# Kernel tuning notes

Measured on AMD Instinct MI355X. Metric: run time of the kernel, lower is better.

The kernel has to match this reference:

```python
import jax, jax.numpy as jnp
import numpy as np

IN_DIM, OUT_DIM = 96, 32
D = IN_DIM + OUT_DIM  # 128, feature dim of x
H, KQ = 8, 64         # head_num, KQ_dim
GAMMA = 1e-4


def setup_inputs() -> dict:
    key = jax.random.key(0)
    kx, kk, kq, kv = jax.random.split(key, 4)
    B, N = 32, 2048
    std_kq = (GAMMA / D) ** 0.5
    return {
        "x": jax.random.normal(kx, (B, N, D), dtype=jnp.float32),
        # nn.Linear weight shape [out_features, in_features]; stacked per head
        "Wk": jax.random.normal(kk, (H, KQ, D), dtype=jnp.float32) * std_kq,
        "Wq": jax.random.normal(kq, (H, KQ, D), dtype=jnp.float32) * std_kq,
        "Wv": jax.random.normal(kv, (H, D, D), dtype=jnp.float32) * GAMMA,
    }


def reference(x, Wk, Wq, Wv):
    # Per-head projections (nn.Linear: y = x @ W^T), stacked over heads h
    K = jnp.einsum("bnd,hkd->bhnk", x, Wk)  # [B,H,N,KQ]
    Q = jnp.einsum("bnd,hkd->bhnk", x, Wq)  # [B,H,N,KQ]
    V = jnp.einsum("bnd,hed->bhne", x, Wv)  # [B,H,N,D]
    # No softmax -> (Q K^T) V == Q (K^T V); use the O(n d^2) associative form
    KtV = jnp.einsum("bhnk,bhne->bhke", K, V)  # [B,H,KQ,D]
    # sum over heads folded into the contraction
    out = jnp.einsum("bhnk,bhke->bne", Q, KtV)  # [B,N,D]
    return out
```

## Files before the change

kernel.cpp:

```cpp
#include <hip/hip_runtime.h>

#define BB 32
#define NN 2048
#define DD 128
#define HH 8
#define KK 64

typedef __attribute__((ext_vector_type(8))) short bf16x8;
typedef __attribute__((ext_vector_type(4))) float f32x4;
#define MFMA_BF16 __builtin_amdgcn_mfma_f32_16x16x32_bf16


__device__ __forceinline__ float bf2f(unsigned short h){ return __uint_as_float(((unsigned)h) << 16); }
__device__ __forceinline__ unsigned short f2bf(float f){
  unsigned u = __float_as_uint(f);
  u += 0x7fffu + ((u >> 16) & 1u);
  return (unsigned short)(u >> 16);
}
__device__ __forceinline__ unsigned pack2(float a, float b){
  return (unsigned)f2bf(a) | ((unsigned)f2bf(b) << 16);
}

__device__ __forceinline__ bf16x8 ldfrag_sw(const unsigned short* base, int row16, int kc, int lane){
  int d = row16 + (lane & 15);
  int q = lane >> 4;
  int ch = ((kc << 2) + q) ^ (d & 7);
  return *(const bf16x8*)(base + d*128 + ch*8);
}

__global__ __launch_bounds__(512, 4) void kgkp(const float* __restrict__ x,
                                               const float* __restrict__ Wq,
                                               const float* __restrict__ Wk,
                                               unsigned short* __restrict__ Gp_bf,
                                               unsigned short* __restrict__ Pbf,
                                               unsigned short* __restrict__ x_bf){
  __shared__ __align__(16) unsigned short sm[32768];
  const int t = threadIdx.x;
  const int bid = blockIdx.x;
  const int w = t >> 6, lane = t & 63, quad = lane >> 4;
  if (bid < 256){
    unsigned short* xh = sm;
    unsigned short* xl = sm + 16384;
    const int b = bid & 31, chunk = bid >> 5;
    const int wr = (w >> 1)*32, wc = (w & 1)*64;
    f32x4 acc[2][4] = {};
    for (int sub = 0; sub < 2; ++sub){
      if (sub) __syncthreads();
      const float* xb = x + ((size_t)b*NN + (size_t)(chunk*256 + sub*128))*DD;
      unsigned short* xbo = x_bf + (((size_t)(b*16 + chunk*2 + sub)) << 14);
      for (int it = 0; it < 2; ++it){
        int gidx = it*512 + t;
        int n4g = (gidx & 7) | (((gidx >> 6) & 3) << 3);
        int dcq = ((gidx >> 3) & 7) | (((gidx >> 8) & 3) << 3);
        float4 v[4];
        #pragma unroll
        for (int j = 0; j < 4; ++j)
          v[j] = *(const float4*)(xb + (size_t)(n4g*4 + j)*DD + dcq*4);
        unsigned short hh[4][4], ll[4][4];
        #pragma unroll
        for (int j = 0; j < 4; ++j)
          #pragma unroll
          for (int i = 0; i < 4; ++i){
            float f = (&v[j].x)[i];
            unsigned short h = f2bf(f);
            hh[j][i] = h;
            ll[j][i] = f2bf(f - bf2f(h));
          }
        #pragma unroll
        for (int i = 0; i < 4; ++i){
          int d = dcq*4 + i;
          int off = d*128 + ((((n4g >> 1) ^ (d & 7)) << 3) + (n4g & 1)*4);
          *(ushort4*)(xh + off) = make_ushort4(hh[0][i], hh[1][i], hh[2][i], hh[3][i]);
          *(ushort4*)(xl + off) = make_ushort4(ll[0][i], ll[1][i], ll[2][i], ll[3][i]);
        }
        #pragma unroll
        for (int j = 0; j < 4; ++j){
          int n = n4g*4 + j;
          int off = n*128 + ((((dcq >> 1) ^ (n & 7)) << 3) + (dcq & 1)*4);
          *(ushort4*)(xbo + off) = make_ushort4(hh[j][0], hh[j][1], hh[j][2], hh[j][3]);
        }
      }
      __syncthreads();
      for (int kc = 0; kc < 4; ++kc){
        bf16x8 ah[2], al[2], bh[4], bl[4];
        #pragma unroll
        for (int r = 0; r < 2; ++r){
          ah[r] = ldfrag_sw(xh, wr + r*16, kc, lane);
          al[r] = ldfrag_sw(xl, wr + r*16, kc, lane);
        }
        #pragma unroll
        for (int c = 0; c < 4; ++c){
          bh[c] = ldfrag_sw(xh, wc + c*16, kc, lane);
          bl[c] = ldfrag_sw(xl, wc + c*16, kc, lane);
        }
        #pragma unroll
        for (int r = 0; r < 2; ++r)
          #pragma unroll
          for (int c = 0; c < 4; ++c){
            acc[r][c] = MFMA_BF16(ah[r], bh[c], acc[r][c], 0, 0, 0);
            acc[r][c] = MFMA_BF16(ah[r], bl[c], acc[r][c], 0, 0, 0);
            acc[r][c] = MFMA_BF16(al[r], bh[c], acc[r][c], 0, 0, 0);
          }
      }
    }
    __syncthreads();
    float* Sf = (float*)sm;
    #pragma unroll
    for (int r = 0; r < 2; ++r)
      #pragma unroll
      for (int c = 0; c < 4; ++c)
        #pragma unroll
        for (int reg = 0; reg < 4; ++reg)
          Sf[(wr + r*16 + quad*4 + reg)*128 + wc + c*16 + (lane & 15)] = acc[r][c][reg];
    __syncthreads();
    unsigned short* gp = Gp_bf + ((size_t)(chunk*32 + b) << 14);
    for (int i = t; i < 2048; i += 512){
      int r = i >> 4, c8 = (i & 15) * 8;
      const float* s = Sf + r*128 + c8;
      uint4 o;
      o.x = pack2(s[0], s[1]); o.y = pack2(s[2], s[3]);
      o.z = pack2(s[4], s[5]); o.w = pack2(s[6], s[7]);
      *(uint4*)(gp + r*128 + c8) = o;
    }
  } else {
    float* Aq = (float*)sm;
    float* Bk = Aq + 64*36;
    const int kpid = bid - 256;
    const int h = kpid >> 2, rt = kpid & 3;
    const int i0 = rt * 32;
    const int tr = t >> 6, tc = t & 63;
    const float* wq = Wq + h*KK*DD;
    const float* wk = Wk + h*KK*DD;
    for (int i = t; i < 512; i += 512){
      int k = i >> 3, c4 = (i & 7) << 2;
      *(float4*)(&Aq[k*36 + c4]) = *(const float4*)(wq + k*DD + i0 + c4);
    }
    for (int i = t; i < 2048; i += 512){
      int k = i >> 5, c4 = (i & 31) << 2;
      *(float4*)(&Bk[k*132 + c4]) = *(const float4*)(wk + k*DD + c4);
    }
    __syncthreads();
    float acc[4][2] = {};
    for (int k = 0; k < 64; k += 2){
      float a0[4], a1[4], b0[2], b1[2];
      *(float4*)a0 = *(float4*)(&Aq[k*36 + tr*4]);
      *(float4*)a1 = *(float4*)(&Aq[(k+1)*36 + tr*4]);
      b0[0] = Bk[k*132 + tc*2];     b0[1] = Bk[k*132 + tc*2 + 1];
      b1[0] = Bk[(k+1)*132 + tc*2]; b1[1] = Bk[(k+1)*132 + tc*2 + 1];
      #pragma unroll
      for (int i = 0; i < 4; ++i)
        #pragma unroll
        for (int j = 0; j < 2; ++j){
          acc[i][j] += a0[i]*b0[j];
          acc[i][j] += a1[i]*b1[j];
        }
    }
    unsigned short* Ph = Pbf + h*DD*DD;
    #pragma unroll
    for (int i = 0; i < 4; ++i){
      int r = i0 + tr*4 + i, c = tc*2;
      int off = r*128 + ((((c >> 3) ^ (r & 7)) << 3) + (c & 7));
      *(ushort2*)(&Ph[off]) = make_ushort2(f2bf(acc[i][0]), f2bf(acc[i][1]));
    }
  }
}

__global__ __launch_bounds__(256) void kgr(const unsigned short* __restrict__ Gp_bf,
                                           const float* __restrict__ Wv,
                                           unsigned short* __restrict__ G_bf,
                                           unsigned short* __restrict__ Wv_bf){
  const int bid = blockIdx.x, t = threadIdx.x;
  if (bid < 256){
    const int b = bid >> 3, strip = bid & 7;
    const int r = strip*16 + (t >> 4), ch = t & 15;
    float s[8] = {};
    #pragma unroll
    for (int p = 0; p < 8; ++p){
      uint4 u = *(const uint4*)(Gp_bf + (((size_t)(p*32 + b)) << 14) + r*128 + ch*8);
      const unsigned short* pu = (const unsigned short*)&u;
      #pragma unroll
      for (int j = 0; j < 8; ++j) s[j] += bf2f(pu[j]);
    }
    uint4 o;
    o.x = pack2(s[0], s[1]); o.y = pack2(s[2], s[3]);
    o.z = pack2(s[4], s[5]); o.w = pack2(s[6], s[7]);
    *(uint4*)(G_bf + ((size_t)b << 14) + r*128 + ((ch ^ (r & 7)) << 3)) = o;
  } else {
    const int h = bid - 256;
    const float* Wvh = Wv + (size_t)h*DD*DD;
    unsigned short* outp = Wv_bf + (size_t)h*DD*DD;
    for (int i = t; i < 4096; i += 256){
      int e = i >> 5, dc = (i & 31) * 4;
      float4 v = *(const float4*)(Wvh + (size_t)e*DD + dc);
      int off = e*128 + ((((dc >> 3) ^ (e & 7)) << 3) + (dc & 4));
      *(ushort4*)(outp + off) = make_ushort4(f2bf(v.x), f2bf(v.y), f2bf(v.z), f2bf(v.w));
    }
  }
}

__global__ __launch_bounds__(512, 2) void km2(const unsigned short* __restrict__ G_bf,
                                              const unsigned short* __restrict__ Wv_bf,
                                              const unsigned short* __restrict__ Pbf,
                                              unsigned short* __restrict__ Mp_bf){
  __shared__ __align__(16) unsigned short sm[32768];
  unsigned short* As = sm;
  unsigned short* Bs = sm + 16384;
  const int bid = blockIdx.x;
  const int b = bid & 31, h = bid >> 5;
  const int t = threadIdx.x;
  const int w = t >> 6, lane = t & 63, quad = lane >> 4;
  const unsigned short* Gb = G_bf + ((size_t)b << 14);
  const unsigned short* Wvh = Wv_bf + ((size_t)h << 14);
  for (int i = t; i < 2048; i += 512){
    *(uint4*)(As + i*8) = *(const uint4*)(Gb + i*8);
    *(uint4*)(Bs + i*8) = *(const uint4*)(Wvh + i*8);
  }
  __syncthreads();
  f32x4 acc1[8] = {};
  for (int kc = 0; kc < 4; ++kc){
    bf16x8 a = ldfrag_sw(As, w*16, kc, lane);
    bf16x8 bb[8];
    #pragma unroll
    for (int c = 0; c < 8; ++c) bb[c] = ldfrag_sw(Bs, c*16, kc, lane);
    #pragma unroll
    for (int c = 0; c < 8; ++c) acc1[c] = MFMA_BF16(a, bb[c], acc1[c], 0, 0, 0);
  }
  __syncthreads();
  #pragma unroll
  for (int c = 0; c < 8; ++c){
    int e = c*16 + (lane & 15);
    int d0 = w*16 + quad*4;
    int off = e*128 + ((((d0 >> 3) ^ (e & 7)) << 3) + (d0 & 7));
    *(ushort4*)(Bs + off) = make_ushort4(f2bf(acc1[c][0]), f2bf(acc1[c][1]),
                                         f2bf(acc1[c][2]), f2bf(acc1[c][3]));
  }
  const unsigned short* Ph = Pbf + (size_t)h*DD*DD;
  for (int i = t; i < 2048; i += 512)
    *(uint4*)(As + i*8) = *(const uint4*)(Ph + i*8);
  __syncthreads();
  f32x4 acc2[8] = {};
  for (int kc = 0; kc < 4; ++kc){
    bf16x8 a = ldfrag_sw(As, w*16, kc, lane);
    bf16x8 bb[8];
    #pragma unroll
    for (int c = 0; c < 8; ++c) bb[c] = ldfrag_sw(Bs, c*16, kc, lane);
    #pragma unroll
    for (int c = 0; c < 8; ++c) acc2[c] = MFMA_BF16(a, bb[c], acc2[c], 0, 0, 0);
  }
  __syncthreads();
  float* Sf = (float*)sm;
  #pragma unroll
  for (int c = 0; c < 8; ++c)
    #pragma unroll
    for (int reg = 0; reg < 4; ++reg)
      Sf[(w*16 + quad*4 + reg)*128 + c*16 + (lane & 15)] = acc2[c][reg];
  __syncthreads();
  unsigned short* Mb = Mp_bf + (((size_t)(b*8 + h)) << 14);
  for (int i = t; i < 2048; i += 512){
    int r = i >> 4, c8 = (i & 15) * 8;
    const float* s = Sf + r*128 + c8;
    uint4 o;
    o.x = pack2(s[0], s[1]); o.y = pack2(s[2], s[3]);
    o.z = pack2(s[4], s[5]); o.w = pack2(s[6], s[7]);
    *(uint4*)(Mb + r*128 + c8) = o;
  }
}

__global__ __launch_bounds__(256) void kmr(const unsigned short* __restrict__ Mp_bf,
                                           unsigned short* __restrict__ Mt_sw){
  __shared__ float Sf[16][132];
  const int bid = blockIdx.x;
  const int b = bid >> 3, es = bid & 7;
  const int t = threadIdx.x;
  {
    int d = t >> 1, half = t & 1;
    float s[8] = {};
    #pragma unroll
    for (int h = 0; h < 8; ++h){
      uint4 u = *(const uint4*)(Mp_bf + (((size_t)(b*8 + h)) << 14) + d*128 + es*16 + half*8);
      const unsigned short* pu = (const unsigned short*)&u;
      #pragma unroll
      for (int j = 0; j < 8; ++j) s[j] += bf2f(pu[j]);
    }
    #pragma unroll
    for (int j = 0; j < 8; ++j) Sf[half*8 + j][d] = s[j];
  }
  __syncthreads();
  unsigned short* Mb = Mt_sw + ((size_t)b << 14);
  {
    int el = t >> 4, ng = t & 15;
    int e = es*16 + el;
    const float* s = &Sf[el][ng*8];
    uint4 o;
    o.x = pack2(s[0], s[1]); o.y = pack2(s[2], s[3]);
    o.z = pack2(s[4], s[5]); o.w = pack2(s[6], s[7]);
    *(uint4*)(Mb + e*128 + ((ng ^ (e & 7)) << 3)) = o;
  }
}

__global__ __launch_bounds__(512, 4) void ko2(const unsigned short* __restrict__ x_bf,
                                              const unsigned short* __restrict__ Mt_sw,
                                              float* __restrict__ out){
  __shared__ __align__(16) unsigned short sm[32768];
  unsigned short* xs = sm;
  unsigned short* Ms = sm + 16384;
  const int bid = blockIdx.x;
  const int b = bid & 31, nt = bid >> 5;
  const int t = threadIdx.x;
  const int w = t >> 6, lane = t & 63, quad = lane >> 4;
  const unsigned short* xbf = x_bf + (((size_t)(b*16 + nt)) << 14);
  const unsigned short* Mtb = Mt_sw + ((size_t)b << 14);
  for (int i = t; i < 2048; i += 512){
    *(uint4*)(xs + i*8) = *(const uint4*)(xbf + i*8);
    *(uint4*)(Ms + i*8) = *(const uint4*)(Mtb + i*8);
  }
  __syncthreads();
  const int wr = (w >> 1)*32, wc = (w & 1)*64;
  f32x4 acc[2][4] = {};
  for (int kc = 0; kc < 4; ++kc){
    bf16x8 a[2], bb[4];
    #pragma unroll
    for (int r = 0; r < 2; ++r) a[r] = ldfrag_sw(xs, wr + r*16, kc, lane);
    #pragma unroll
    for (int c = 0; c < 4; ++c) bb[c] = ldfrag_sw(Ms, wc + c*16, kc, lane);
    #pragma unroll
    for (int r = 0; r < 2; ++r)
      #pragma unroll
      for (int c = 0; c < 4; ++c)
        acc[r][c] = MFMA_BF16(a[r], bb[c], acc[r][c], 0, 0, 0);
  }
  __syncthreads();
  float* Sf = (float*)sm;
  #pragma unroll
  for (int r = 0; r < 2; ++r)
    #pragma unroll
    for (int c = 0; c < 4; ++c)
      #pragma unroll
      for (int reg = 0; reg < 4; ++reg)
        Sf[(wr + r*16 + quad*4 + reg)*128 + wc + c*16 + (lane & 15)] = acc[r][c][reg];
  __syncthreads();
  float* ob = out + ((size_t)b*NN + (size_t)nt*128)*DD;
  for (int i = t; i < 4096; i += 512){
    int n = i >> 5, c4 = (i & 31) * 4;
    *(float4*)(ob + (size_t)n*DD + c4) = *(const float4*)(Sf + n*128 + c4);
  }
}

extern "C" void kernel_launch(void* const* d_in, const int* in_sizes, int n_in,
                              void* d_out, int out_size, void* d_ws, size_t ws_size,
                              hipStream_t stream){
  const float* x  = (const float*)d_in[0];
  const float* Wk = (const float*)d_in[1];
  const float* Wq = (const float*)d_in[2];
  const float* Wv = (const float*)d_in[3];
  float* out = (float*)d_out;
  unsigned short* wsu = (unsigned short*)d_ws;
  unsigned short* Gp_bf = wsu;
  unsigned short* G_bf  = wsu + 4194304;
  unsigned short* Pbf   = wsu + 4718592;
  unsigned short* Wv_bf = wsu + 4849664;
  unsigned short* Mp_bf = wsu + 4980736;
  unsigned short* Mt_sw = wsu + 9175040;
  unsigned short* x_bf  = wsu + 9699328;

  kgkp<<<288, 512, 0, stream>>>(x, Wq, Wk, Gp_bf, Pbf, x_bf);
  kgr <<<264, 256, 0, stream>>>(Gp_bf, Wv, G_bf, Wv_bf);
  km2 <<<256, 512, 0, stream>>>(G_bf, Wv_bf, Pbf, Mp_bf);
  kmr <<<256, 256, 0, stream>>>(Mp_bf, Mt_sw);
  ko2 <<<512, 512, 0, stream>>>(x_bf, Mt_sw, out);
}
```

Measured before the change: 126.2 us.

## Fuse Gram reduce, M computation and output GEMM into one kernel

Replaces the kgr, km2, kmr and ko2 kernels with a single kernel in which each block reduces the partial Gram for its batch, loops over all heads to accumulate M in registers (double-buffering Wv and P tiles through registers), then applies M to two x tiles. Wv bf16 conversion moves into the first kernel. This removes three launches and the global round trips of G, Mp and Mt, at the cost of recomputing M redundantly in every block for a batch and larger shared memory use.

Measured after the change: 153.4 us. 1.22x slower.

```diff
diff --git a/kernel.cpp b/kernel.cpp
--- a/kernel.cpp
+++ b/kernel.cpp
@@ -1,9 +1,7 @@
 #include <hip/hip_runtime.h>
 
-#define BB 32
 #define NN 2048
 #define DD 128
-#define HH 8
 #define KK 64
 
 typedef __attribute__((ext_vector_type(8))) short bf16x8;
@@ -31,8 +29,10 @@
 __global__ __launch_bounds__(512, 4) void kgkp(const float* __restrict__ x,
                                                const float* __restrict__ Wq,
                                                const float* __restrict__ Wk,
+                                               const float* __restrict__ Wv,
                                                unsigned short* __restrict__ Gp_bf,
                                                unsigned short* __restrict__ Pbf,
+                                               unsigned short* __restrict__ Wv_bf,
                                                unsigned short* __restrict__ x_bf){
   __shared__ __align__(16) unsigned short sm[32768];
   const int t = threadIdx.x;
@@ -129,6 +129,17 @@
     const int h = kpid >> 2, rt = kpid & 3;
     const int i0 = rt * 32;
     const int tr = t >> 6, tc = t & 63;
+    {
+      const float* wvh = Wv + (size_t)h*DD*DD;
+      unsigned short* wvo = Wv_bf + (size_t)h*16384;
+      for (int i = t; i < 1024; i += 512){
+        int el = i >> 5, dc = (i & 31)*4;
+        int e = i0 + el;
+        float4 v = *(const float4*)(wvh + (size_t)e*DD + dc);
+        int off = e*128 + ((((dc >> 3) ^ (e & 7)) << 3) + (dc & 4));
+        *(ushort4*)(wvo + off) = make_ushort4(f2bf(v.x), f2bf(v.y), f2bf(v.z), f2bf(v.w));
+      }
+    }
     const float* wq = Wq + h*KK*DD;
     const float* wk = Wk + h*KK*DD;
     for (int i = t; i < 512; i += 512){
@@ -165,18 +176,32 @@
   }
 }
 
-__global__ __launch_bounds__(256) void kgr(const unsigned short* __restrict__ Gp_bf,
-                                           const float* __restrict__ Wv,
-                                           unsigned short* __restrict__ G_bf,
-                                           unsigned short* __restrict__ Wv_bf){
-  const int bid = blockIdx.x, t = threadIdx.x;
-  if (bid < 256){
-    const int b = bid >> 3, strip = bid & 7;
-    const int r = strip*16 + (t >> 4), ch = t & 15;
+__global__ __launch_bounds__(512, 2) void kall(const unsigned short* __restrict__ Gp_bf,
+                                               const unsigned short* __restrict__ Wv_bf,
+                                               const unsigned short* __restrict__ Pbf,
+                                               const unsigned short* __restrict__ x_bf,
+                                               float* __restrict__ out){
+  __shared__ __align__(16) unsigned short sm[49152];
+  unsigned short* Gs = sm;
+  unsigned short* Ps = sm + 16384;
+  unsigned short* Bs = sm + 32768;
+  const int bid = blockIdx.x;
+  const int b = bid & 31, ntg = bid >> 5;
+  const int t = threadIdx.x;
+  const int w = t >> 6, lane = t & 63, quad = lane >> 4;
+
+  uint4 wreg[4], preg[4];
+  #pragma unroll
+  for (int r = 0; r < 4; ++r){
+    wreg[r] = *(const uint4*)(Wv_bf + (size_t)(r*512 + t)*8);
+    preg[r] = *(const uint4*)(Pbf   + (size_t)(r*512 + t)*8);
+  }
+  for (int i = t; i < 2048; i += 512){
+    int r = i >> 4, c8 = (i & 15) * 8;
     float s[8] = {};
     #pragma unroll
     for (int p = 0; p < 8; ++p){
-      uint4 u = *(const uint4*)(Gp_bf + (((size_t)(p*32 + b)) << 14) + r*128 + ch*8);
+      uint4 u = *(const uint4*)(Gp_bf + (((size_t)(p*32 + b)) << 14) + r*128 + c8);
       const unsigned short* pu = (const unsigned short*)&u;
       #pragma unroll
       for (int j = 0; j < 8; ++j) s[j] += bf2f(pu[j]);
@@ -184,165 +209,112 @@
     uint4 o;
     o.x = pack2(s[0], s[1]); o.y = pack2(s[2], s[3]);
     o.z = pack2(s[4], s[5]); o.w = pack2(s[6], s[7]);
-    *(uint4*)(G_bf + ((size_t)b << 14) + r*128 + ((ch ^ (r & 7)) << 3)) = o;
-  } else {
-    const int h = bid - 256;
-    const float* Wvh = Wv + (size_t)h*DD*DD;
-    unsigned short* outp = Wv_bf + (size_t)h*DD*DD;
-    for (int i = t; i < 4096; i += 256){
-      int e = i >> 5, dc = (i & 31) * 4;
-      float4 v = *(const float4*)(Wvh + (size_t)e*DD + dc);
-      int off = e*128 + ((((dc >> 3) ^ (e & 7)) << 3) + (dc & 4));
-      *(ushort4*)(outp + off) = make_ushort4(f2bf(v.x), f2bf(v.y), f2bf(v.z), f2bf(v.w));
-    }
-  }
-}
-
-__global__ __launch_bounds__(512, 2) void km2(const unsigned short* __restrict__ G_bf,
-                                              const unsigned short* __restrict__ Wv_bf,
-                                              const unsigned short* __restrict__ Pbf,
-                                              unsigned short* __restrict__ Mp_bf){
-  __shared__ __align__(16) unsigned short sm[32768];
-  unsigned short* As = sm;
-  unsigned short* Bs = sm + 16384;
-  const int bid = blockIdx.x;
-  const int b = bid & 31, h = bid >> 5;
-  const int t = threadIdx.x;
-  const int w = t >> 6, lane = t & 63, quad = lane >> 4;
-  const unsigned short* Gb = G_bf + ((size_t)b << 14);
-  const unsigned short* Wvh = Wv_bf + ((size_t)h << 14);
-  for (int i = t; i < 2048; i += 512){
-    *(uint4*)(As + i*8) = *(const uint4*)(Gb + i*8);
-    *(uint4*)(Bs + i*8) = *(const uint4*)(Wvh + i*8);
+    *(uint4*)(Gs + r*128 + ((((c8 >> 3) ^ (r & 7))) << 3)) = o;
+  }
+  #pragma unroll
+  for (int r = 0; r < 4; ++r){
+    *(uint4*)(Bs + (r*512 + t)*8) = wreg[r];
+    *(uint4*)(Ps + (r*512 + t)*8) = preg[r];
+  }
+  #pragma unroll
+  for (int r = 0; r < 4; ++r){
+    wreg[r] = *(const uint4*)(Wv_bf + 16384 + (size_t)(r*512 + t)*8);
+    preg[r] = *(const uint4*)(Pbf   + 16384 + (size_t)(r*512 + t)*8);
   }
   __syncthreads();
-  f32x4 acc1[8] = {};
-  for (int kc = 0; kc < 4; ++kc){
-    bf16x8 a = ldfrag_sw(As, w*16, kc, lane);
-    bf16x8 bb[8];
-    #pragma unroll
-    for (int c = 0; c < 8; ++c) bb[c] = ldfrag_sw(Bs, c*16, kc, lane);
-    #pragma unroll
-    for (int c = 0; c < 8; ++c) acc1[c] = MFMA_BF16(a, bb[c], acc1[c], 0, 0, 0);
-  }
-  __syncthreads();
+
+  f32x4 macc[8] = {};
+  for (int h = 0; h < 8; ++h){
+    f32x4 acc1[8] = {};
+    for (int kc = 0; kc < 4; ++kc){
+      bf16x8 a = ldfrag_sw(Gs, w*16, kc, lane);
+      bf16x8 bb[8];
+      #pragma unroll
+      for (int c = 0; c < 8; ++c) bb[c] = ldfrag_sw(Bs, c*16, kc, lane);
+      #pragma unroll
+      for (int c = 0; c < 8; ++c) acc1[c] = MFMA_BF16(a, bb[c], acc1[c], 0, 0, 0);
+    }
+    __syncthreads();
+    #pragma unroll
+    for (int c = 0; c < 8; ++c){
+      int e = c*16 + (lane & 15);
+      int d0 = w*16 + quad*4;
+      int off = e*128 + ((((d0 >> 3) ^ (e & 7)) << 3) + (d0 & 7));
+      *(ushort4*)(Bs + off) = make_ushort4(f2bf(acc1[c][0]), f2bf(acc1[c][1]),
+                                           f2bf(acc1[c][2]), f2bf(acc1[c][3]));
+    }
+    __syncthreads();
+    for (int kc = 0; kc < 4; ++kc){
+      bf16x8 a = ldfrag_sw(Ps, w*16, kc, lane);
+      bf16x8 bb[8];
+      #pragma unroll
+      for (int c = 0; c < 8; ++c) bb[c] = ldfrag_sw(Bs, c*16, kc, lane);
+      #pragma unroll
+      for (int c = 0; c < 8; ++c) macc[c] = MFMA_BF16(a, bb[c], macc[c], 0, 0, 0);
+    }
+    __syncthreads();
+    if (h < 7){
+      #pragma unroll
+      for (int r = 0; r < 4; ++r){
+        *(uint4*)(Bs + (r*512 + t)*8) = wreg[r];
+        *(uint4*)(Ps + (r*512 + t)*8) = preg[r];
+      }
+      if (h < 6){
+        #pragma unroll
+        for (int r = 0; r < 4; ++r){
+          wreg[r] = *(const uint4*)(Wv_bf + (size_t)(h+2)*16384 + (size_t)(r*512 + t)*8);
+          preg[r] = *(const uint4*)(Pbf   + (size_t)(h+2)*16384 + (size_t)(r*512 + t)*8);
+        }
+      }
+      __syncthreads();
+    }
+  }
   #pragma unroll
   for (int c = 0; c < 8; ++c){
     int e = c*16 + (lane & 15);
     int d0 = w*16 + quad*4;
     int off = e*128 + ((((d0 >> 3) ^ (e & 7)) << 3) + (d0 & 7));
-    *(ushort4*)(Bs + off) = make_ushort4(f2bf(acc1[c][0]), f2bf(acc1[c][1]),
-                                         f2bf(acc1[c][2]), f2bf(acc1[c][3]));
-  }
-  const unsigned short* Ph = Pbf + (size_t)h*DD*DD;
-  for (int i = t; i < 2048; i += 512)
-    *(uint4*)(As + i*8) = *(const uint4*)(Ph + i*8);
+    *(ushort4*)(Bs + off) = make_ushort4(f2bf(macc[c][0]), f2bf(macc[c][1]),
+                                         f2bf(macc[c][2]), f2bf(macc[c][3]));
+  }
   __syncthreads();
-  f32x4 acc2[8] = {};
-  for (int kc = 0; kc < 4; ++kc){
-    bf16x8 a = ldfrag_sw(As, w*16, kc, lane);
-    bf16x8 bb[8];
-    #pragma unroll
-    for (int c = 0; c < 8; ++c) bb[c] = ldfrag_sw(Bs, c*16, kc, lane);
-    #pragma unroll
-    for (int c = 0; c < 8; ++c) acc2[c] = MFMA_BF16(a, bb[c], acc2[c], 0, 0, 0);
-  }
-  __syncthreads();
-  float* Sf = (float*)sm;
-  #pragma unroll
-  for (int c = 0; c < 8; ++c)
-    #pragma unroll
-    for (int reg = 0; reg < 4; ++reg)
-      Sf[(w*16 + quad*4 + reg)*128 + c*16 + (lane & 15)] = acc2[c][reg];
-  __syncthreads();
-  unsigned short* Mb = Mp_bf + (((size_t)(b*8 + h)) << 14);
-  for (int i = t; i < 2048; i += 512){
-    int r = i >> 4, c8 = (i & 15) * 8;
-    const float* s = Sf + r*128 + c8;
-    uint4 o;
-    o.x = pack2(s[0], s[1]); o.y = pack2(s[2], s[3]);
-    o.z = pack2(s[4], s[5]); o.w = pack2(s[6], s[7]);
-    *(uint4*)(Mb + r*128 + c8) = o;
-  }
-}
-
-__global__ __launch_bounds__(256) void kmr(const unsigned short* __restrict__ Mp_bf,
-                                           unsigned short* __restrict__ Mt_sw){
-  __shared__ float Sf[16][132];
-  const int bid = blockIdx.x;
-  const int b = bid >> 3, es = bid & 7;
-  const int t = threadIdx.x;
-  {
-    int d = t >> 1, half = t & 1;
-    float s[8] = {};
-    #pragma unroll
-    for (int h = 0; h < 8; ++h){
-      uint4 u = *(const uint4*)(Mp_bf + (((size_t)(b*8 + h)) << 14) + d*128 + es*16 + half*8);
-      const unsigned short* pu = (const unsigned short*)&u;
-      #pragma unroll
-      for (int j = 0; j < 8; ++j) s[j] += bf2f(pu[j]);
-    }
-    #pragma unroll
-    for (int j = 0; j < 8; ++j) Sf[half*8 + j][d] = s[j];
-  }
-  __syncthreads();
-  unsigned short* Mb = Mt_sw + ((size_t)b << 14);
-  {
-    int el = t >> 4, ng = t & 15;
-    int e = es*16 + el;
-    const float* s = &Sf[el][ng*8];
-    uint4 o;
-    o.x = pack2(s[0], s[1]); o.y = pack2(s[2], s[3]);
-    o.z = pack2(s[4], s[5]); o.w = pack2(s[6], s[7]);
-    *(uint4*)(Mb + e*128 + ((ng ^ (e & 7)) << 3)) = o;
-  }
-}
-
-__global__ __launch_bounds__(512, 4) void ko2(const unsigned short* __restrict__ x_bf,
-                                              const unsigned short* __restrict__ Mt_sw,
-                                              float* __restrict__ out){
-  __shared__ __align__(16) unsigned short sm[32768];
-  unsigned short* xs = sm;
-  unsigned short* Ms = sm + 16384;
-  const int bid = blockIdx.x;
-  const int b = bid & 31, nt = bid >> 5;
-  const int t = threadIdx.x;
-  const int w = t >> 6, lane = t & 63, quad = lane >> 4;
-  const unsigned short* xbf = x_bf + (((size_t)(b*16 + nt)) << 14);
-  const unsigned short* Mtb = Mt_sw + ((size_t)b << 14);
-  for (int i = t; i < 2048; i += 512){
-    *(uint4*)(xs + i*8) = *(const uint4*)(xbf + i*8);
-    *(uint4*)(Ms + i*8) = *(const uint4*)(Mtb + i*8);
-  }
-  __syncthreads();
+
   const int wr = (w >> 1)*32, wc = (w & 1)*64;
-  f32x4 acc[2][4] = {};
-  for (int kc = 0; kc < 4; ++kc){
-    bf16x8 a[2], bb[4];
-    #pragma unroll
-    for (int r = 0; r < 2; ++r) a[r] = ldfrag_sw(xs, wr + r*16, kc, lane);
-    #pragma unroll
-    for (int c = 0; c < 4; ++c) bb[c] = ldfrag_sw(Ms, wc + c*16, kc, lane);
+  for (int i2 = 0; i2 < 2; ++i2){
+    int nt = ntg*2 + i2;
+    const unsigned short* xbf = x_bf + (((size_t)(b*16 + nt)) << 14);
+    for (int i = t; i < 2048; i += 512)
+      *(uint4*)(Gs + i*8) = *(const uint4*)(xbf + i*8);
+    __syncthreads();
+    f32x4 acc[2][4] = {};
+    for (int kc = 0; kc < 4; ++kc){
+      bf16x8 a[2], bb[4];
+      #pragma unroll
+      for (int r = 0; r < 2; ++r) a[r] = ldfrag_sw(Gs, wr + r*16, kc, lane);
+      #pragma unroll
+      for (int c = 0; c < 4; ++c) bb[c] = ldfrag_sw(Bs, wc + c*16, kc, lane);
+      #pragma unroll
+      for (int r = 0; r < 2; ++r)
+        #pragma unroll
+        for (int c = 0; c < 4; ++c)
+          acc[r][c] = MFMA_BF16(a[r], bb[c], acc[r][c], 0, 0, 0);
+    }
+    __syncthreads();
+    float* Sf = (float*)sm;
     #pragma unroll
     for (int r = 0; r < 2; ++r)
       #pragma unroll
       for (int c = 0; c < 4; ++c)
-        acc[r][c] = MFMA_BF16(a[r], bb[c], acc[r][c], 0, 0, 0);
-  }
-  __syncthreads();
-  float* Sf = (float*)sm;
-  #pragma unroll
-  for (int r = 0; r < 2; ++r)
-    #pragma unroll
-    for (int c = 0; c < 4; ++c)
-      #pragma unroll
-      for (int reg = 0; reg < 4; ++reg)
-        Sf[(wr + r*16 + quad*4 + reg)*128 + wc + c*16 + (lane & 15)] = acc[r][c][reg];
-  __syncthreads();
-  float* ob = out + ((size_t)b*NN + (size_t)nt*128)*DD;
-  for (int i = t; i < 4096; i += 512){
-    int n = i >> 5, c4 = (i & 31) * 4;
-    *(float4*)(ob + (size_t)n*DD + c4) = *(const float4*)(Sf + n*128 + c4);
+        #pragma unroll
+        for (int reg = 0; reg < 4; ++reg)
+          Sf[(wr + r*16 + quad*4 + reg)*128 + wc + c*16 + (lane & 15)] = acc[r][c][reg];
+    __syncthreads();
+    float* ob = out + ((size_t)b*NN + (size_t)nt*128)*DD;
+    for (int i = t; i < 4096; i += 512){
+      int n = i >> 5, c4 = (i & 31) * 4;
+      *(float4*)(ob + (size_t)n*DD + c4) = *(const float4*)(Sf + n*128 + c4);
+    }
+    if (i2 == 0) __syncthreads();
   }
 }
 
@@ -356,16 +328,10 @@
   float* out = (float*)d_out;
   unsigned short* wsu = (unsigned short*)d_ws;
   unsigned short* Gp_bf = wsu;
-  unsigned short* G_bf  = wsu + 4194304;
-  unsigned short* Pbf   = wsu + 4718592;
-  unsigned short* Wv_bf = wsu + 4849664;
-  unsigned short* Mp_bf = wsu + 4980736;
-  unsigned short* Mt_sw = wsu + 9175040;
-  unsigned short* x_bf  = wsu + 9699328;
-
-  kgkp<<<288, 512, 0, stream>>>(x, Wq, Wk, Gp_bf, Pbf, x_bf);
-  kgr <<<264, 256, 0, stream>>>(Gp_bf, Wv, G_bf, Wv_bf);
-  km2 <<<256, 512, 0, stream>>>(G_bf, Wv_bf, Pbf, Mp_bf);
-  kmr <<<256, 256, 0, stream>>>(Mp_bf, Mt_sw);
-  ko2 <<<512, 512, 0, stream>>>(x_bf, Mt_sw, out);
-}
+  unsigned short* Pbf   = wsu + 4194304;
+  unsigned short* Wv_bf = wsu + 4325376;
+  unsigned short* x_bf  = wsu + 4456448;
+
+  kgkp<<<288, 512, 0, stream>>>(x, Wq, Wk, Wv, Gp_bf, Pbf, Wv_bf, x_bf);
+  kall<<<256, 512, 0, stream>>>(Gp_bf, Wv_bf, Pbf, x_bf, out);
+}
```
